# Kernel optimization log

Hardware: AMD Instinct MI355X
Metric: run time of the kernel (lower is better)

## Reference

```python
import jax, jax.numpy as jnp
import numpy as np

NUM_HEADS = 16
KEY_DEPTH = 1024


def setup_inputs() -> dict:
    key = jax.random.key(0)
    ks = jax.random.split(key, 7)
    B, L, D = 2, 2048, 1024
    scale = 1.0 / np.sqrt(D)
    return {
        "query_antecedent": jax.random.normal(ks[0], (B, L, D), jnp.float32),
        "memory_antecedent": jax.random.normal(ks[1], (B, L, D), jnp.float32),
        "bias": jax.random.normal(ks[2], (1, 1, L, L), jnp.float32),
        "Wq": jax.random.normal(ks[3], (D, KEY_DEPTH), jnp.float32) * scale,
        "Wk": jax.random.normal(ks[4], (D, KEY_DEPTH), jnp.float32) * scale,
        "Wv": jax.random.normal(ks[5], (D, KEY_DEPTH), jnp.float32) * scale,
        "Wo": jax.random.normal(ks[6], (KEY_DEPTH, D), jnp.float32) * scale,
    }


def _split_heads(x, h):
    # [B, L, D] -> [B, H, L, D/H]
    b, l, d = x.shape
    return x.reshape(b, l, h, d // h).transpose(0, 2, 1, 3)


def reference(query_antecedent, memory_antecedent, bias, Wq, Wk, Wv, Wo):
    h = NUM_HEADS
    d_head = KEY_DEPTH // h
    q = _split_heads(query_antecedent @ Wq, h) * (d_head ** -0.5)
    k = _split_heads(memory_antecedent @ Wk, h)
    v = _split_heads(memory_antecedent @ Wv, h)
    # [B, H, Lq, Lk]
    logits = jnp.einsum("bhqd,bhkd->bhqk", q, k) + bias
    weights = jax.nn.softmax(logits, axis=-1)
    x = jnp.einsum("bhqk,bhkd->bhqd", weights, v)
    # combine heads: [B, H, L, d] -> [B, L, H*d]
    b, _, l, d = x.shape
    x = x.transpose(0, 2, 1, 3).reshape(b, l, h * d)
    return x @ Wo
```

## Files before the change

### kernel.cpp

```cpp
#include <hip/hip_runtime.h>
#include <hip/hip_bf16.h>


typedef __attribute__((ext_vector_type(8))) short short8;
typedef __attribute__((ext_vector_type(4))) short short4v;
typedef __attribute__((ext_vector_type(4))) float float4v;

#define BATCH 2
#define LSEQ 2048
#define DMODEL 1024
#define NHEADS 16
#define DHEAD 64
#define MROWS 4096
#define QKVLD 3072

__global__ __launch_bounds__(256)
void convert_kernel(const float* __restrict__ qa, const float* __restrict__ ma,
                    __hip_bfloat16* __restrict__ qo, __hip_bfloat16* __restrict__ mo)
{
    const size_t i = ((size_t)blockIdx.x * 256 + threadIdx.x) * 8;
    const float* src = blockIdx.y ? ma : qa;
    __hip_bfloat16* dst = blockIdx.y ? mo : qo;
    float4 v0 = *reinterpret_cast<const float4*>(src + i);
    float4 v1 = *reinterpret_cast<const float4*>(src + i + 4);
    union { __hip_bfloat16 h[8]; int4 v; } pk;
    pk.h[0] = (__hip_bfloat16)v0.x; pk.h[1] = (__hip_bfloat16)v0.y;
    pk.h[2] = (__hip_bfloat16)v0.z; pk.h[3] = (__hip_bfloat16)v0.w;
    pk.h[4] = (__hip_bfloat16)v1.x; pk.h[5] = (__hip_bfloat16)v1.y;
    pk.h[6] = (__hip_bfloat16)v1.z; pk.h[7] = (__hip_bfloat16)v1.w;
    *reinterpret_cast<int4*>(dst + i) = pk.v;
}

__global__ __launch_bounds__(256)
void transpose_w_kernel(const float* __restrict__ W0, const float* __restrict__ W1,
                        const float* __restrict__ W2, const float* __restrict__ W3,
                        __hip_bfloat16* __restrict__ T0, __hip_bfloat16* __restrict__ T1,
                        __hip_bfloat16* __restrict__ T2, __hip_bfloat16* __restrict__ T3)
{
    __shared__ __hip_bfloat16 T[64][68];

    const float* W; __hip_bfloat16* D;
    if      (blockIdx.z == 0) { W = W0; D = T0; }
    else if (blockIdx.z == 1) { W = W1; D = T1; }
    else if (blockIdx.z == 2) { W = W2; D = T2; }
    else                      { W = W3; D = T3; }

    const int t  = threadIdx.x;
    const int n0 = blockIdx.x * 64;
    const int k0 = blockIdx.y * 64;

#pragma unroll
    for (int p = 0; p < 4; ++p) {
        const int r = p * 16 + (t >> 4);
        const int c = (t & 15) * 4;
        float4 v = *reinterpret_cast<const float4*>(&W[(size_t)(k0 + r) * DMODEL + n0 + c]);
        union { __hip_bfloat16 h[4]; ushort4 v; } pk;
        pk.h[0] = (__hip_bfloat16)v.x; pk.h[1] = (__hip_bfloat16)v.y;
        pk.h[2] = (__hip_bfloat16)v.z; pk.h[3] = (__hip_bfloat16)v.w;
        *reinterpret_cast<ushort4*>(&T[r][c]) = pk.v;
    }
    __syncthreads();
#pragma unroll
    for (int p = 0; p < 2; ++p) {
        const int n  = p * 32 + (t & 31);
        const int kc = (t >> 5) * 8;
        union { __hip_bfloat16 h[8]; int4 v; } pk;
#pragma unroll
        for (int j = 0; j < 8; ++j) pk.h[j] = T[kc + j][n];
        *reinterpret_cast<int4*>(&D[(size_t)(n0 + n) * DMODEL + k0 + kc]) = pk.v;
    }
}

__global__ __launch_bounds__(256)
void gemm_bt_kernel(const __hip_bfloat16* __restrict__ A0,
                    const __hip_bfloat16* __restrict__ A1, int nsplit,
                    float alpha0, float alpha1,
                    const __hip_bfloat16* __restrict__ Bt,
                    float* __restrict__ Cf, __hip_bfloat16* __restrict__ Cb,
                    int K, int ldc)
{
    __shared__ __hip_bfloat16 As[128][40];
    __shared__ __hip_bfloat16 Bs[128][40];

    const int t    = threadIdx.x;
    const int w    = t >> 6;
    const int lane = t & 63;
    const int l15  = lane & 15;
    const int lq   = lane >> 4;
    const int m0   = blockIdx.y * 128;
    const int n0   = blockIdx.x * 128;
    const int wm   = (w >> 1) * 64;
    const int wn   = (w & 1) * 64;
    const int sr   = t >> 1;
    const int sc   = (t & 1) * 16;

    const __hip_bfloat16* A = (n0 < nsplit) ? A0 : A1;
    const float alpha = (n0 < nsplit) ? alpha0 : alpha1;

    float4v acc[4][4];
#pragma unroll
    for (int mi = 0; mi < 4; ++mi)
#pragma unroll
        for (int ni = 0; ni < 4; ++ni) acc[mi][ni] = (float4v){0.f, 0.f, 0.f, 0.f};

    const __hip_bfloat16* Arow = A  + (size_t)(m0 + sr) * K + sc;
    const __hip_bfloat16* Brow = Bt + (size_t)(n0 + sr) * K + sc;

    int4 a0 = *reinterpret_cast<const int4*>(Arow);
    int4 a1 = *reinterpret_cast<const int4*>(Arow + 8);
    int4 b0 = *reinterpret_cast<const int4*>(Brow);
    int4 b1 = *reinterpret_cast<const int4*>(Brow + 8);

    for (int k0 = 0; k0 < K; k0 += 32) {
        __syncthreads();
        *reinterpret_cast<int4*>(&As[sr][sc])     = a0;
        *reinterpret_cast<int4*>(&As[sr][sc + 8]) = a1;
        *reinterpret_cast<int4*>(&Bs[sr][sc])     = b0;
        *reinterpret_cast<int4*>(&Bs[sr][sc + 8]) = b1;
        const int kn = (k0 + 32 < K) ? k0 + 32 : k0;
        a0 = *reinterpret_cast<const int4*>(Arow + kn);
        a1 = *reinterpret_cast<const int4*>(Arow + kn + 8);
        b0 = *reinterpret_cast<const int4*>(Brow + kn);
        b1 = *reinterpret_cast<const int4*>(Brow + kn + 8);
        __syncthreads();

        short8 af[4], bf[4];
#pragma unroll
        for (int mi = 0; mi < 4; ++mi)
            af[mi] = *reinterpret_cast<const short8*>(&As[wm + mi * 16 + l15][lq * 8]);
#pragma unroll
        for (int ni = 0; ni < 4; ++ni)
            bf[ni] = *reinterpret_cast<const short8*>(&Bs[wn + ni * 16 + l15][lq * 8]);
#pragma unroll
        for (int mi = 0; mi < 4; ++mi)
#pragma unroll
            for (int ni = 0; ni < 4; ++ni)
                acc[mi][ni] = __builtin_amdgcn_mfma_f32_16x16x32_bf16(
                    af[mi], bf[ni], acc[mi][ni], 0, 0, 0);
    }

#pragma unroll
    for (int mi = 0; mi < 4; ++mi)
#pragma unroll
        for (int ni = 0; ni < 4; ++ni)
#pragma unroll
            for (int r = 0; r < 4; ++r) {
                const int row = m0 + wm + mi * 16 + lq * 4 + r;
                const int col = n0 + wn + ni * 16 + l15;
                const float v = acc[mi][ni][r] * alpha;
                if (Cf) Cf[(size_t)row * ldc + col] = v;
                else    Cb[(size_t)row * ldc + col] = (__hip_bfloat16)v;
            }
}

#define KSTR 68
#define PSTR 132

__global__ __launch_bounds__(256)
void attn_mfma_kernel(const __hip_bfloat16* __restrict__ QKV,
                      const float* __restrict__ bias,
                      __hip_bfloat16* __restrict__ X)
{
    __shared__ __hip_bfloat16 Ks[128][KSTR];
    __shared__ __hip_bfloat16 Vt[64][PSTR];

    const int t   = threadIdx.x;
    const int w   = t >> 6;
    const int l15 = t & 15;
    const int lq  = (t & 63) >> 4;

    const int bid = blockIdx.x;
    const int r8  = bid & 7;
    const int j   = bid >> 3;
    const int bh  = r8 + 8 * (j >> 4);
    const int q0  = (j & 15) * 128;
    const int b   = bh >> 4;
    const int h   = bh & 15;

    const __hip_bfloat16* Kb = QKV + (size_t)b * LSEQ * QKVLD + 1024 + h * DHEAD;
    const __hip_bfloat16* Vb = Kb + 1024;

    short8 aq[2][2];
#pragma unroll
    for (int g = 0; g < 2; ++g) {
        const __hip_bfloat16* qrow = QKV +
            (size_t)(b * LSEQ + q0 + w * 32 + g * 16 + l15) * QKVLD + h * DHEAD + lq * 8;
        aq[g][0] = *reinterpret_cast<const short8*>(qrow);
        aq[g][1] = *reinterpret_cast<const short8*>(qrow + 32);
    }

    const float* bp0 = bias + (size_t)(q0 + w * 32 + l15) * LSEQ + lq * 4;
    const float* bp1 = bp0 + (size_t)16 * LSEQ;

    float lsum[2] = {0.f, 0.f};
    float4v o_acc[2][4];
#pragma unroll
    for (int g = 0; g < 2; ++g)
#pragma unroll
        for (int n = 0; n < 4; ++n) o_acc[g][n] = (float4v){0.f, 0.f, 0.f, 0.f};

    const int skey = t >> 2;
    const int sdh  = (t & 3) * 16;
    const int g2   = t & 3;

    int4 pk[2][2], pv[2][2];
#pragma unroll
    for (int rnd = 0; rnd < 2; ++rnd) {
        const int key = rnd * 64 + skey;
        const __hip_bfloat16* ks = Kb + (size_t)key * QKVLD + sdh;
        pk[rnd][0] = *reinterpret_cast<const int4*>(ks);
        pk[rnd][1] = *reinterpret_cast<const int4*>(ks + 8);
        const __hip_bfloat16* vs = Vb + (size_t)key * QKVLD + sdh;
        pv[rnd][0] = *reinterpret_cast<const int4*>(vs);
        pv[rnd][1] = *reinterpret_cast<const int4*>(vs + 8);
    }

    for (int kt = 0; kt < LSEQ / 128; ++kt) {
        const int k0 = kt * 128;
        __syncthreads();
#pragma unroll
        for (int rnd = 0; rnd < 2; ++rnd) {
            const int key = rnd * 64 + skey;
            *reinterpret_cast<int4*>(&Ks[key][sdh])     = pk[rnd][0];
            *reinterpret_cast<int4*>(&Ks[key][sdh + 8]) = pk[rnd][1];
            const __hip_bfloat16* vp0 = reinterpret_cast<const __hip_bfloat16*>(&pv[rnd][0]);
            const __hip_bfloat16* vp1 = reinterpret_cast<const __hip_bfloat16*>(&pv[rnd][1]);
            const int vcol = (((key >> 3) ^ g2) << 3) + (key & 7);
#pragma unroll
            for (int jj = 0; jj < 8; ++jj) Vt[sdh + jj][vcol]     = vp0[jj];
#pragma unroll
            for (int jj = 0; jj < 8; ++jj) Vt[sdh + 8 + jj][vcol] = vp1[jj];
        }
        {
            const int knext = (kt + 1 < LSEQ / 128) ? k0 + 128 : k0;
#pragma unroll
            for (int rnd = 0; rnd < 2; ++rnd) {
                const int key = knext + rnd * 64 + skey;
                const __hip_bfloat16* ks = Kb + (size_t)key * QKVLD + sdh;
                pk[rnd][0] = *reinterpret_cast<const int4*>(ks);
                pk[rnd][1] = *reinterpret_cast<const int4*>(ks + 8);
                const __hip_bfloat16* vs = Vb + (size_t)key * QKVLD + sdh;
                pv[rnd][0] = *reinterpret_cast<const int4*>(vs);
                pv[rnd][1] = *reinterpret_cast<const int4*>(vs + 8);
            }
        }
        __syncthreads();

#pragma unroll
        for (int m = 0; m < 4; ++m) {
            short8 bkA0 = *reinterpret_cast<const short8*>(&Ks[(2*m)    *16 + l15][lq * 8]);
            short8 bkA1 = *reinterpret_cast<const short8*>(&Ks[(2*m)    *16 + l15][32 + lq * 8]);
            short8 bkB0 = *reinterpret_cast<const short8*>(&Ks[(2*m + 1)*16 + l15][lq * 8]);
            short8 bkB1 = *reinterpret_cast<const short8*>(&Ks[(2*m + 1)*16 + l15][32 + lq * 8]);
            float4v sA[2], sB[2];
#pragma unroll
            for (int g = 0; g < 2; ++g) {
                sA[g] = (float4v){0.f, 0.f, 0.f, 0.f};
                sB[g] = (float4v){0.f, 0.f, 0.f, 0.f};
            }
            __builtin_amdgcn_s_setprio(1);
#pragma unroll
            for (int g = 0; g < 2; ++g) {
                sA[g] = __builtin_amdgcn_mfma_f32_16x16x32_bf16(bkA0, aq[g][0], sA[g], 0, 0, 0);
                sA[g] = __builtin_amdgcn_mfma_f32_16x16x32_bf16(bkA1, aq[g][1], sA[g], 0, 0, 0);
                sB[g] = __builtin_amdgcn_mfma_f32_16x16x32_bf16(bkB0, aq[g][0], sB[g], 0, 0, 0);
                sB[g] = __builtin_amdgcn_mfma_f32_16x16x32_bf16(bkB1, aq[g][1], sB[g], 0, 0, 0);
            }
            __builtin_amdgcn_s_setprio(0);

            short8 pf[2];
#pragma unroll
            for (int g = 0; g < 2; ++g) {
                const float* bp = g ? bp1 : bp0;
                float4v bvA = *reinterpret_cast<const float4v*>(bp + k0 + (2*m)     * 16);
                float4v bvB = *reinterpret_cast<const float4v*>(bp + k0 + (2*m + 1) * 16);
                union { __hip_bfloat16 hh[8]; short8 v; } pp;
#pragma unroll
                for (int r = 0; r < 4; ++r) {
                    const float e = __expf(sA[g][r] + bvA[r]);
                    lsum[g] += e;
                    pp.hh[r] = (__hip_bfloat16)e;
                }
#pragma unroll
                for (int r = 0; r < 4; ++r) {
                    const float e = __expf(sB[g][r] + bvB[r]);
                    lsum[g] += e;
                    pp.hh[4 + r] = (__hip_bfloat16)e;
                }
                pf[g] = pp.v;
            }

            short8 vt[4];
#pragma unroll
            for (int n = 0; n < 4; ++n) {
                const int c0 = (((4*m +     (lq >> 1)) ^ n) << 3) + ((lq & 1) << 2);
                const int c1 = (((4*m + 2 + (lq >> 1)) ^ n) << 3) + ((lq & 1) << 2);
                union { short4v h[2]; short8 v; } u;
                u.h[0] = *reinterpret_cast<const short4v*>(&Vt[n * 16 + l15][c0]);
                u.h[1] = *reinterpret_cast<const short4v*>(&Vt[n * 16 + l15][c1]);
                vt[n] = u.v;
            }
            __builtin_amdgcn_s_setprio(1);
#pragma unroll
            for (int g = 0; g < 2; ++g)
#pragma unroll
                for (int n = 0; n < 4; ++n)
                    o_acc[g][n] = __builtin_amdgcn_mfma_f32_16x16x32_bf16(
                        vt[n], pf[g], o_acc[g][n], 0, 0, 0);
            __builtin_amdgcn_s_setprio(0);
        }
    }

#pragma unroll
    for (int g = 0; g < 2; ++g) {
        lsum[g] += __shfl_xor(lsum[g], 16);
        lsum[g] += __shfl_xor(lsum[g], 32);
        const float inv = 1.f / lsum[g];
        const int row = q0 + w * 32 + g * 16 + l15;
        __hip_bfloat16* dst = X + (size_t)(b * LSEQ + row) * DMODEL + h * DHEAD + lq * 4;
#pragma unroll
        for (int n = 0; n < 4; ++n) {
            union { __hip_bfloat16 hh[4]; short4v v; } o;
#pragma unroll
            for (int r = 0; r < 4; ++r) o.hh[r] = (__hip_bfloat16)(o_acc[g][n][r] * inv);
            *reinterpret_cast<short4v*>(dst + n * 16) = o.v;
        }
    }
}

extern "C" void kernel_launch(void* const* d_in, const int* in_sizes, int n_in,
                              void* d_out, int out_size, void* d_ws, size_t ws_size,
                              hipStream_t stream)
{
    const float* qa   = (const float*)d_in[0];
    const float* ma   = (const float*)d_in[1];
    const float* bias = (const float*)d_in[2];
    const float* Wq   = (const float*)d_in[3];
    const float* Wk   = (const float*)d_in[4];
    const float* Wv   = (const float*)d_in[5];
    const float* Wo   = (const float*)d_in[6];
    float* out = (float*)d_out;

    char* wsb = (char*)d_ws;
    __hip_bfloat16* qa16 = (__hip_bfloat16*)(wsb);
    __hip_bfloat16* ma16 = (__hip_bfloat16*)(wsb + (8u << 20));
    __hip_bfloat16* Wt   = (__hip_bfloat16*)(wsb + (16u << 20));
    __hip_bfloat16* Wot  = (__hip_bfloat16*)(wsb + (22u << 20));
    __hip_bfloat16* QKVw = (__hip_bfloat16*)(wsb + (24u << 20));
    __hip_bfloat16* Xw   = qa16;

    convert_kernel<<<dim3(MROWS * DMODEL / (256 * 8), 2), 256, 0, stream>>>(
        qa, ma, qa16, ma16);

    transpose_w_kernel<<<dim3(16, 16, 4), 256, 0, stream>>>(
        Wq, Wk, Wv, Wo,
        Wt, Wt + (size_t)DMODEL * DMODEL, Wt + 2 * (size_t)DMODEL * DMODEL, Wot);

    gemm_bt_kernel<<<dim3(QKVLD / 128, MROWS / 128), 256, 0, stream>>>(
        qa16, ma16, DMODEL, 0.125f, 1.0f, Wt, nullptr, QKVw, DMODEL, QKVLD);

    attn_mfma_kernel<<<dim3(512), 256, 0, stream>>>(QKVw, bias, Xw);

    gemm_bt_kernel<<<dim3(DMODEL / 128, MROWS / 128), 256, 0, stream>>>(
        Xw, Xw, DMODEL + 1, 1.0f, 1.0f, Wot, out, nullptr, DMODEL, DMODEL);
}
```

Before: 287.5 us.

## Use 512-thread attention blocks with one 16-row query group per wave

The attention kernel now launches 512 threads (8 waves) per block. Each wave handles 16 query rows instead of 32, so the per-thread accumulators, Q fragments and softmax sums are halved, and each thread stages one K/V row per tile instead of two. The V transpose swizzle is redesigned so each lane reads V with a single 16-byte LDS load instead of two 8-byte loads. Lower register pressure and more waves per CU should improve latency hiding, at the cost of each K/V tile in LDS being reused by fewer query rows per wave and more barrier participants.

Result: faster. 246.0 us (-14.4%).

```diff
diff --git a/kernel.cpp b/kernel.cpp
--- a/kernel.cpp
+++ b/kernel.cpp
@@ -156,7 +156,7 @@
 #define KSTR 68
 #define PSTR 132
 
-__global__ __launch_bounds__(256)
+__global__ __launch_bounds__(512, 4)
 void attn_mfma_kernel(const __hip_bfloat16* __restrict__ QKV,
                       const float* __restrict__ bias,
                       __hip_bfloat16* __restrict__ X)
@@ -180,52 +180,45 @@
     const __hip_bfloat16* Kb = QKV + (size_t)b * LSEQ * QKVLD + 1024 + h * DHEAD;
     const __hip_bfloat16* Vb = Kb + 1024;
 
-    short8 aq[2][2];
-#pragma unroll
-    for (int g = 0; g < 2; ++g) {
+    short8 aq[2];
+    {
         const __hip_bfloat16* qrow = QKV +
-            (size_t)(b * LSEQ + q0 + w * 32 + g * 16 + l15) * QKVLD + h * DHEAD + lq * 8;
-        aq[g][0] = *reinterpret_cast<const short8*>(qrow);
-        aq[g][1] = *reinterpret_cast<const short8*>(qrow + 32);
-    }
-
-    const float* bp0 = bias + (size_t)(q0 + w * 32 + l15) * LSEQ + lq * 4;
-    const float* bp1 = bp0 + (size_t)16 * LSEQ;
-
-    float lsum[2] = {0.f, 0.f};
-    float4v o_acc[2][4];
-#pragma unroll
-    for (int g = 0; g < 2; ++g)
-#pragma unroll
-        for (int n = 0; n < 4; ++n) o_acc[g][n] = (float4v){0.f, 0.f, 0.f, 0.f};
+            (size_t)(b * LSEQ + q0 + w * 16 + l15) * QKVLD + h * DHEAD + lq * 8;
+        aq[0] = *reinterpret_cast<const short8*>(qrow);
+        aq[1] = *reinterpret_cast<const short8*>(qrow + 32);
+    }
+
+    const float* bp = bias + (size_t)(q0 + w * 16 + l15) * LSEQ + lq * 4;
+
+    float lsum = 0.f;
+    float4v o_acc[4];
+#pragma unroll
+    for (int n = 0; n < 4; ++n) o_acc[n] = (float4v){0.f, 0.f, 0.f, 0.f};
 
     const int skey = t >> 2;
     const int sdh  = (t & 3) * 16;
-    const int g2   = t & 3;
-
-    int4 pk[2][2], pv[2][2];
-#pragma unroll
-    for (int rnd = 0; rnd < 2; ++rnd) {
-        const int key = rnd * 64 + skey;
-        const __hip_bfloat16* ks = Kb + (size_t)key * QKVLD + sdh;
-        pk[rnd][0] = *reinterpret_cast<const int4*>(ks);
-        pk[rnd][1] = *reinterpret_cast<const int4*>(ks + 8);
-        const __hip_bfloat16* vs = Vb + (size_t)key * QKVLD + sdh;
-        pv[rnd][0] = *reinterpret_cast<const int4*>(vs);
-        pv[rnd][1] = *reinterpret_cast<const int4*>(vs + 8);
+    const int a    = t & 3;
+    const int cblk = ((skey >> 5) << 2) | ((skey >> 2) & 3);
+    const int vcol = (((cblk ^ a) << 3)) | ((((skey >> 4) & 1) << 2)) | (skey & 3);
+
+    int4 pk0, pk1, pv0, pv1;
+    {
+        const __hip_bfloat16* ks = Kb + (size_t)skey * QKVLD + sdh;
+        pk0 = *reinterpret_cast<const int4*>(ks);
+        pk1 = *reinterpret_cast<const int4*>(ks + 8);
+        const __hip_bfloat16* vs = Vb + (size_t)skey * QKVLD + sdh;
+        pv0 = *reinterpret_cast<const int4*>(vs);
+        pv1 = *reinterpret_cast<const int4*>(vs + 8);
     }
 
     for (int kt = 0; kt < LSEQ / 128; ++kt) {
         const int k0 = kt * 128;
         __syncthreads();
-#pragma unroll
-        for (int rnd = 0; rnd < 2; ++rnd) {
-            const int key = rnd * 64 + skey;
-            *reinterpret_cast<int4*>(&Ks[key][sdh])     = pk[rnd][0];
-            *reinterpret_cast<int4*>(&Ks[key][sdh + 8]) = pk[rnd][1];
-            const __hip_bfloat16* vp0 = reinterpret_cast<const __hip_bfloat16*>(&pv[rnd][0]);
-            const __hip_bfloat16* vp1 = reinterpret_cast<const __hip_bfloat16*>(&pv[rnd][1]);
-            const int vcol = (((key >> 3) ^ g2) << 3) + (key & 7);
+        *reinterpret_cast<int4*>(&Ks[skey][sdh])     = pk0;
+        *reinterpret_cast<int4*>(&Ks[skey][sdh + 8]) = pk1;
+        {
+            const __hip_bfloat16* vp0 = reinterpret_cast<const __hip_bfloat16*>(&pv0);
+            const __hip_bfloat16* vp1 = reinterpret_cast<const __hip_bfloat16*>(&pv1);
 #pragma unroll
             for (int jj = 0; jj < 8; ++jj) Vt[sdh + jj][vcol]     = vp0[jj];
 #pragma unroll
@@ -233,16 +226,12 @@
         }
         {
             const int knext = (kt + 1 < LSEQ / 128) ? k0 + 128 : k0;
-#pragma unroll
-            for (int rnd = 0; rnd < 2; ++rnd) {
-                const int key = knext + rnd * 64 + skey;
-                const __hip_bfloat16* ks = Kb + (size_t)key * QKVLD + sdh;
-                pk[rnd][0] = *reinterpret_cast<const int4*>(ks);
-                pk[rnd][1] = *reinterpret_cast<const int4*>(ks + 8);
-                const __hip_bfloat16* vs = Vb + (size_t)key * QKVLD + sdh;
-                pv[rnd][0] = *reinterpret_cast<const int4*>(vs);
-                pv[rnd][1] = *reinterpret_cast<const int4*>(vs + 8);
-            }
+            const __hip_bfloat16* ks = Kb + (size_t)(knext + skey) * QKVLD + sdh;
+            pk0 = *reinterpret_cast<const int4*>(ks);
+            pk1 = *reinterpret_cast<const int4*>(ks + 8);
+            const __hip_bfloat16* vs = Vb + (size_t)(knext + skey) * QKVLD + sdh;
+            pv0 = *reinterpret_cast<const int4*>(vs);
+            pv1 = *reinterpret_cast<const int4*>(vs + 8);
         }
         __syncthreads();
 
@@ -252,77 +241,59 @@
             short8 bkA1 = *reinterpret_cast<const short8*>(&Ks[(2*m)    *16 + l15][32 + lq * 8]);
             short8 bkB0 = *reinterpret_cast<const short8*>(&Ks[(2*m + 1)*16 + l15][lq * 8]);
             short8 bkB1 = *reinterpret_cast<const short8*>(&Ks[(2*m + 1)*16 + l15][32 + lq * 8]);
-            float4v sA[2], sB[2];
-#pragma unroll
-            for (int g = 0; g < 2; ++g) {
-                sA[g] = (float4v){0.f, 0.f, 0.f, 0.f};
-                sB[g] = (float4v){0.f, 0.f, 0.f, 0.f};
+            float4v bvA = *reinterpret_cast<const float4v*>(bp + k0 + 32 * m);
+            float4v bvB = *reinterpret_cast<const float4v*>(bp + k0 + 32 * m + 16);
+
+            float4v sA = (float4v){0.f, 0.f, 0.f, 0.f};
+            float4v sB = (float4v){0.f, 0.f, 0.f, 0.f};
+            __builtin_amdgcn_s_setprio(1);
+            sA = __builtin_amdgcn_mfma_f32_16x16x32_bf16(bkA0, aq[0], sA, 0, 0, 0);
+            sA = __builtin_amdgcn_mfma_f32_16x16x32_bf16(bkA1, aq[1], sA, 0, 0, 0);
+            sB = __builtin_amdgcn_mfma_f32_16x16x32_bf16(bkB0, aq[0], sB, 0, 0, 0);
+            sB = __builtin_amdgcn_mfma_f32_16x16x32_bf16(bkB1, aq[1], sB, 0, 0, 0);
+            __builtin_amdgcn_s_setprio(0);
+
+            union { __hip_bfloat16 hh[8]; short8 v; } pp;
+#pragma unroll
+            for (int r = 0; r < 4; ++r) {
+                const float e = __expf(sA[r] + bvA[r]);
+                lsum += e;
+                pp.hh[r] = (__hip_bfloat16)e;
             }
+#pragma unroll
+            for (int r = 0; r < 4; ++r) {
+                const float e = __expf(sB[r] + bvB[r]);
+                lsum += e;
+                pp.hh[4 + r] = (__hip_bfloat16)e;
+            }
+            const short8 pf = pp.v;
+
+            short8 vt[4];
+#pragma unroll
+            for (int n = 0; n < 4; ++n)
+                vt[n] = *reinterpret_cast<const short8*>(
+                    &Vt[n * 16 + l15][((m * 4 + lq) ^ n) << 3]);
+
             __builtin_amdgcn_s_setprio(1);
 #pragma unroll
-            for (int g = 0; g < 2; ++g) {
-                sA[g] = __builtin_amdgcn_mfma_f32_16x16x32_bf16(bkA0, aq[g][0], sA[g], 0, 0, 0);
-                sA[g] = __builtin_amdgcn_mfma_f32_16x16x32_bf16(bkA1, aq[g][1], sA[g], 0, 0, 0);
-                sB[g] = __builtin_amdgcn_mfma_f32_16x16x32_bf16(bkB0, aq[g][0], sB[g], 0, 0, 0);
-                sB[g] = __builtin_amdgcn_mfma_f32_16x16x32_bf16(bkB1, aq[g][1], sB[g], 0, 0, 0);
-            }
-            __builtin_amdgcn_s_setprio(0);
-
-            short8 pf[2];
-#pragma unroll
-            for (int g = 0; g < 2; ++g) {
-                const float* bp = g ? bp1 : bp0;
-                float4v bvA = *reinterpret_cast<const float4v*>(bp + k0 + (2*m)     * 16);
-                float4v bvB = *reinterpret_cast<const float4v*>(bp + k0 + (2*m + 1) * 16);
-                union { __hip_bfloat16 hh[8]; short8 v; } pp;
-#pragma unroll
-                for (int r = 0; r < 4; ++r) {
-                    const float e = __expf(sA[g][r] + bvA[r]);
-                    lsum[g] += e;
-                    pp.hh[r] = (__hip_bfloat16)e;
-                }
-#pragma unroll
-                for (int r = 0; r < 4; ++r) {
-                    const float e = __expf(sB[g][r] + bvB[r]);
-                    lsum[g] += e;
-                    pp.hh[4 + r] = (__hip_bfloat16)e;
-                }
-                pf[g] = pp.v;
-            }
-
-            short8 vt[4];
-#pragma unroll
-            for (int n = 0; n < 4; ++n) {
-                const int c0 = (((4*m +     (lq >> 1)) ^ n) << 3) + ((lq & 1) << 2);
-                const int c1 = (((4*m + 2 + (lq >> 1)) ^ n) << 3) + ((lq & 1) << 2);
-                union { short4v h[2]; short8 v; } u;
-                u.h[0] = *reinterpret_cast<const short4v*>(&Vt[n * 16 + l15][c0]);
-                u.h[1] = *reinterpret_cast<const short4v*>(&Vt[n * 16 + l15][c1]);
-                vt[n] = u.v;
-            }
-            __builtin_amdgcn_s_setprio(1);
-#pragma unroll
-            for (int g = 0; g < 2; ++g)
-#pragma unroll
-                for (int n = 0; n < 4; ++n)
-                    o_acc[g][n] = __builtin_amdgcn_mfma_f32_16x16x32_bf16(
-                        vt[n], pf[g], o_acc[g][n], 0, 0, 0);
+            for (int n = 0; n < 4; ++n)
+                o_acc[n] = __builtin_amdgcn_mfma_f32_16x16x32_bf16(
+                    vt[n], pf, o_acc[n], 0, 0, 0);
             __builtin_amdgcn_s_setprio(0);
         }
     }
 
-#pragma unroll
-    for (int g = 0; g < 2; ++g) {
-        lsum[g] += __shfl_xor(lsum[g], 16);
-        lsum[g] += __shfl_xor(lsum[g], 32);
-        const float inv = 1.f / lsum[g];
-        const int row = q0 + w * 32 + g * 16 + l15;
+    lsum += __shfl_xor(lsum, 16);
+    lsum += __shfl_xor(lsum, 32);
+    const float inv = 1.f / lsum;
+    {
+        const int row = q0 + w * 16 + l15;
         __hip_bfloat16* dst = X + (size_t)(b * LSEQ + row) * DMODEL + h * DHEAD + lq * 4;
 #pragma unroll
         for (int n = 0; n < 4; ++n) {
             union { __hip_bfloat16 hh[4]; short4v v; } o;
 #pragma unroll
-            for (int r = 0; r < 4; ++r) o.hh[r] = (__hip_bfloat16)(o_acc[g][n][r] * inv);
+            for (int r = 0; r < 4; ++r) o.hh[r] = (__hip_bfloat16)(o_acc[n][r] * inv);
             *reinterpret_cast<short4v*>(dst + n * 16) = o.v;
         }
     }
@@ -359,7 +330,7 @@
     gemm_bt_kernel<<<dim3(QKVLD / 128, MROWS / 128), 256, 0, stream>>>(
         qa16, ma16, DMODEL, 0.125f, 1.0f, Wt, nullptr, QKVw, DMODEL, QKVLD);
 
-    attn_mfma_kernel<<<dim3(512), 256, 0, stream>>>(QKVw, bias, Xw);
+    attn_mfma_kernel<<<dim3(512), 512, 0, stream>>>(QKVw, bias, Xw);
 
     gemm_bt_kernel<<<dim3(DMODEL / 128, MROWS / 128), 256, 0, stream>>>(
         Xw, Xw, DMODEL + 1, 1.0f, 1.0f, Wot, out, nullptr, DMODEL, DMODEL);
```
